# Performance work log

Hardware: AMD Instinct MI355X
Metric: run time of the kernel (lower is better)

Reference implementation:

```python
import jax, jax.numpy as jnp
import numpy as np

B, T, D = 4, 2048, 1024
GROUPS = 32
EPS = 1e-5
THETA = 10000.0


def _rope(x):
    # lucidrains RotaryEmbedding: interleaved pairs over the full dim
    d = x.shape[-1]
    t = x.shape[-2]
    inv_freq = 1.0 / (THETA ** (jnp.arange(0, d, 2, dtype=jnp.float32) / d))  # [d/2]
    freqs = jnp.arange(t, dtype=jnp.float32)[:, None] * inv_freq[None, :]      # [T, d/2]
    cos = jnp.cos(freqs).astype(x.dtype)
    sin = jnp.sin(freqs).astype(x.dtype)
    x1 = x[..., 0::2]
    x2 = x[..., 1::2]
    r1 = x1 * cos - x2 * sin
    r2 = x1 * sin + x2 * cos
    return jnp.stack([r1, r2], axis=-1).reshape(x.shape)


def _group_norm(z, weight, bias):
    # z: [N, C]; normalize per group of C//GROUPS channels
    n, c = z.shape
    zg = z.reshape(n, GROUPS, c // GROUPS)
    mean = zg.mean(axis=-1, keepdims=True)
    var = zg.var(axis=-1, keepdims=True)
    zg = (zg - mean) * jax.lax.rsqrt(var + EPS)
    return zg.reshape(n, c) * weight + bias


def setup_inputs() -> dict:
    key = jax.random.key(0)
    k1, k2, k3 = jax.random.split(key, 3)
    x = jax.random.normal(k1, (B, T, D), dtype=jnp.float32)
    W_in = jax.random.normal(k2, (D, 3 * D), dtype=jnp.float32) * (1.0 / np.sqrt(D))
    b_in = jax.random.normal(k3, (3 * D,), dtype=jnp.float32) * 0.02
    gn_weight = jnp.ones((D,), dtype=jnp.float32)
    gn_bias = jnp.zeros((D,), dtype=jnp.float32)
    return {"x": x, "W_in": W_in, "b_in": b_in, "gn_weight": gn_weight, "gn_bias": gn_bias}


def reference(x, W_in, b_in, gn_weight, gn_bias):
    b, t, c = x.shape
    qkv = x @ W_in + b_in                    # [B,T,3D]
    Q, K, V = jnp.split(qkv, 3, axis=-1)
    Q = jax.nn.relu(_rope(Q))
    K = jax.nn.relu(_rope(K))
    V = jax.nn.relu(V)
    A = jnp.einsum('btd,bsd->bts', Q, K)     # [B,T,T], no softmax
    y = jnp.einsum('bts,bsd->btd', A, V)     # [B,T,D]
    y = _group_norm(y.reshape(-1, c), gn_weight, gn_bias).reshape(b, t, c)
    # faithful to original: transpose(-2,-1).reshape(B,T,dim)
    return jnp.swapaxes(y, -2, -1).reshape(b, t, c)
```

## Files before the change

### kernel.cpp

```cpp
#include <hip/hip_runtime.h>


typedef unsigned short u16;
typedef __attribute__((ext_vector_type(8))) unsigned short u16x8;
typedef __attribute__((ext_vector_type(4))) float fx4;
typedef __attribute__((ext_vector_type(8))) __bf16 bfx8;

#define TP 129

__device__ __forceinline__ u16 f2bh(float v) {
  unsigned u = __float_as_uint(v);
  return (u16)((u + 0x7FFFu + ((u >> 16) & 1u)) >> 16);
}
__device__ __forceinline__ fx4 mfma16(bfx8 a, bfx8 b, fx4 c) {
  return __builtin_amdgcn_mfma_f32_16x16x32_bf16(a, b, c, 0, 0, 0);
}

__device__ __forceinline__ void gload16(const u16* g, u16* l) {
  __builtin_amdgcn_global_load_lds(
      (const __attribute__((address_space(1))) unsigned int*)(const void*)g,
      (__attribute__((address_space(3))) unsigned int*)(void*)l, 16, 0, 0);
}

__device__ __forceinline__ bfx8 ldsw(const u16* lds, int row, int slot) {
  const char* p = (const char*)lds + row * 128 + ((slot ^ (row & 7)) << 4);
  return __builtin_bit_cast(bfx8, *reinterpret_cast<const u16x8*>(p));
}

__device__ __forceinline__ void stage4(const u16* __restrict__ A,
                                       size_t rowBase, int stride, int k0,
                                       u16* lds, int w, int lane) {
#pragma unroll
  for (int i = 0; i < 4; ++i) {
    int c = ((w * 4 + i) << 6) + lane;
    int r = c >> 3, s = c & 7;
    int t = s ^ (r & 7);
    const u16* src = A + (rowBase + (size_t)r) * (size_t)stride + k0 + (t << 3);
    gload16(src, lds + ((w * 4 + i) << 9));
  }
}

__device__ inline void gemm_core_pipe(const u16* __restrict__ A, size_t aBase, int aStr,
                                      const u16* __restrict__ B, size_t bBase, int bStr, int K,
                                      u16* sA0, u16* sB0, u16* sA1, u16* sB1,
                                      fx4 acc[4][4], int w, int lane) {
  int wm = (w >> 1) * 64, wn = (w & 1) * 64;
  int lr = lane & 15, lk = lane >> 4;
  stage4(A, aBase, aStr, 0, sA0, w, lane);
  stage4(B, bBase, bStr, 0, sB0, w, lane);
  int NT = K >> 6;
  for (int t = 0; t < NT; ++t) {
    u16* cA = (t & 1) ? sA1 : sA0;
    u16* cB = (t & 1) ? sB1 : sB0;
    if (t + 1 < NT) {
      u16* nA = (t & 1) ? sA0 : sA1;
      u16* nB = (t & 1) ? sB0 : sB1;
      stage4(A, aBase, aStr, (t + 1) << 6, nA, w, lane);
      stage4(B, bBase, bStr, (t + 1) << 6, nB, w, lane);
      asm volatile("s_waitcnt vmcnt(8)" ::: "memory");
    } else {
      asm volatile("s_waitcnt vmcnt(0)" ::: "memory");
    }
    __builtin_amdgcn_s_barrier();
    __builtin_amdgcn_sched_barrier(0);
    bfx8 a[8], b[8];
#pragma unroll
    for (int h = 0; h < 2; ++h)
#pragma unroll
      for (int i = 0; i < 4; ++i) {
        a[h * 4 + i] = ldsw(cA, wm + i * 16 + lr, h * 4 + lk);
        b[h * 4 + i] = ldsw(cB, wn + i * 16 + lr, h * 4 + lk);
      }
    asm volatile("s_waitcnt lgkmcnt(0)" ::: "memory");
    __builtin_amdgcn_sched_barrier(0);
    __builtin_amdgcn_s_barrier();
#pragma unroll
    for (int h = 0; h < 2; ++h)
#pragma unroll
      for (int mi = 0; mi < 4; ++mi)
#pragma unroll
        for (int ni = 0; ni < 4; ++ni)
          acc[mi][ni] = mfma16(a[h * 4 + mi], b[h * 4 + ni], acc[mi][ni]);
  }
}

__global__ void k_ropetab(float2* __restrict__ tabTI, float2* __restrict__ tabIT) {
  int idx = blockIdx.x * 256 + threadIdx.x;
  int t, i;
  if (blockIdx.y == 0) {
    t = idx >> 9;
    i = idx & 511;
  } else {
    i = idx >> 11;
    t = idx & 2047;
  }
  float invf = exp2f(-(float)i * (13.287712379549449f / 512.f));
  float ang = (float)t * invf, s, c;
  sincosf(ang, &s, &c);
  if (blockIdx.y == 0)
    tabTI[idx] = make_float2(c, s);
  else
    tabIT[idx] = make_float2(c, s);
}

__global__ void k_transW(const float* __restrict__ W, u16* __restrict__ WTh) {
  __shared__ float tile[32][33];
  int n0 = blockIdx.x * 32, k0 = blockIdx.y * 32;
  int tid = threadIdx.x;
  int c = tid & 31, r4 = tid >> 5;
#pragma unroll
  for (int it = 0; it < 4; ++it) {
    int r = r4 + it * 8;
    tile[r][c] = W[(size_t)(k0 + r) * 3072 + n0 + c];
  }
  __syncthreads();
#pragma unroll
  for (int it = 0; it < 4; ++it) {
    int r = r4 + it * 8;
    WTh[(size_t)(n0 + r) * 1024 + k0 + c] = f2bh(tile[c][r]);
  }
}

__global__ void k_castX(const float* __restrict__ x, u16* __restrict__ xh) {
  size_t i = ((size_t)blockIdx.x * 256 + threadIdx.x) * 8;
  fx4 v0 = *reinterpret_cast<const fx4*>(x + i);
  fx4 v1 = *reinterpret_cast<const fx4*>(x + i + 4);
  u16x8 h;
#pragma unroll
  for (int j = 0; j < 4; ++j) {
    h[j] = f2bh(v0[j]);
    h[4 + j] = f2bh(v1[j]);
  }
  *reinterpret_cast<u16x8*>(xh + i) = h;
}

__global__ __launch_bounds__(256) void k_gemm1f(const u16* __restrict__ xh,
                                                const u16* __restrict__ WTh,
                                                const float* __restrict__ b_in,
                                                const float2* __restrict__ tabTI,
                                                const float2* __restrict__ tabIT,
                                                u16* __restrict__ Qh, u16* __restrict__ Kth,
                                                u16* __restrict__ Vth) {
  __shared__ __align__(16) float shbuf[128 * TP];
  u16* sA0 = (u16*)shbuf;
  u16* sB0 = sA0 + 128 * 64;
  u16* sA1 = sB0 + 128 * 64;
  u16* sB1 = sA1 + 128 * 64;
  int bid = blockIdx.x;
  int xcd = bid & 7, idx = bid >> 3;
  int mt = (xcd << 3) + (idx & 7), nt = idx >> 3;
  int m0 = mt << 7, n0 = nt << 7;
  int tid = threadIdx.x, lane = tid & 63, w = tid >> 6;
  int wm = (w >> 1) * 64, wn = (w & 1) * 64;
  int lr = lane & 15, lk = lane >> 4;
  fx4 acc[4][4];
#pragma unroll
  for (int i = 0; i < 4; ++i)
#pragma unroll
    for (int j = 0; j < 4; ++j) acc[i][j] = fx4{0.f, 0.f, 0.f, 0.f};

  gemm_core_pipe(xh, (size_t)m0, 1024, WTh, (size_t)n0, 1024, 1024,
                 sA0, sB0, sA1, sB1, acc, w, lane);

  float bv[4];
#pragma unroll
  for (int ni = 0; ni < 4; ++ni) bv[ni] = b_in[n0 + wn + ni * 16 + lr];
  __syncthreads();
#pragma unroll
  for (int mi = 0; mi < 4; ++mi)
#pragma unroll
    for (int ni = 0; ni < 4; ++ni)
#pragma unroll
      for (int r = 0; r < 4; ++r)
        shbuf[(wn + ni * 16 + lr) * TP + wm + mi * 16 + lk * 4 + r] = acc[mi][ni][r] + bv[ni];
  __syncthreads();

  int part = n0 >> 10;
  int d0 = n0 - (part << 10);
  int bb = m0 >> 11, tb = m0 & 2047;
  int rl0 = tid >> 4;
  int cc = (tid & 15) * 8;

  if (part == 2) {
#pragma unroll
    for (int pass = 0; pass < 8; ++pass) {
      int rl = rl0 + pass * 16;
      u16x8 o;
#pragma unroll
      for (int j = 0; j < 8; ++j) o[j] = f2bh(fmaxf(shbuf[rl * TP + cc + j], 0.f));
      *reinterpret_cast<u16x8*>(Vth + (((size_t)(bb << 10) + d0 + rl) << 11) + tb + cc) = o;
    }
  } else if (part == 1) {
#pragma unroll
    for (int pass = 0; pass < 8; ++pass) {
      int rl = rl0 + pass * 16;
      int d = d0 + rl;
      const float2* tp = tabIT + ((size_t)(d >> 1) << 11) + tb + cc;
      const float* e = shbuf + (rl & ~1) * TP + cc;
      const float* oo = shbuf + (rl | 1) * TP + cc;
      int isOdd = d & 1;
      u16x8 o;
#pragma unroll
      for (int j = 0; j < 8; ++j) {
        float2 cs = tp[j];
        float x1 = e[j], x2 = oo[j];
        float v = isOdd ? (x1 * cs.y + x2 * cs.x) : (x1 * cs.x - x2 * cs.y);
        o[j] = f2bh(fmaxf(v, 0.f));
      }
      *reinterpret_cast<u16x8*>(Kth + (((size_t)(bb << 10) + d) << 11) + tb + cc) = o;
    }
  } else {
#pragma unroll
    for (int pass = 0; pass < 8; ++pass) {
      int rl = rl0 + pass * 16;
      int m = m0 + rl, t = m & 2047;
      const float2* tp = tabTI + ((size_t)t << 9) + ((d0 + cc) >> 1);
      u16x8 o;
#pragma unroll
      for (int jp = 0; jp < 4; ++jp) {
        float x1 = shbuf[(cc + 2 * jp) * TP + rl];
        float x2 = shbuf[(cc + 2 * jp + 1) * TP + rl];
        float2 cs = tp[jp];
        o[2 * jp] = f2bh(fmaxf(x1 * cs.x - x2 * cs.y, 0.f));
        o[2 * jp + 1] = f2bh(fmaxf(x1 * cs.y + x2 * cs.x, 0.f));
      }
      *reinterpret_cast<u16x8*>(Qh + ((size_t)m << 10) + d0 + cc) = o;
    }
  }
}

__global__ __launch_bounds__(256) void k_gemm2(const u16* __restrict__ Kth, const u16* __restrict__ Vth,
                                               u16* __restrict__ KtVTh) {
  __shared__ u16 smem[4 * 128 * 64];
  u16* sA0 = smem;
  u16* sB0 = sA0 + 128 * 64;
  u16* sA1 = sB0 + 128 * 64;
  u16* sB1 = sA1 + 128 * 64;
  fx4 acc[4][4];
#pragma unroll
  for (int i = 0; i < 4; ++i)
#pragma unroll
    for (int j = 0; j < 4; ++j) acc[i][j] = fx4{0.f, 0.f, 0.f, 0.f};
  int b = blockIdx.z;
  int m0 = blockIdx.x << 7, n0 = blockIdx.y << 7;
  int tid = threadIdx.x, lane = tid & 63, w = tid >> 6;
  const u16* Ab = Kth + ((size_t)b << 21);
  const u16* Bb = Vth + ((size_t)b << 21);
  gemm_core_pipe(Ab, (size_t)m0, 2048, Bb, (size_t)n0, 2048, 2048,
                 sA0, sB0, sA1, sB1, acc, w, lane);
  int wm = (w >> 1) * 64, wn = (w & 1) * 64, lr = lane & 15, lk = lane >> 4;
#pragma unroll
  for (int mi = 0; mi < 4; ++mi)
#pragma unroll
    for (int ni = 0; ni < 4; ++ni)
#pragma unroll
      for (int r = 0; r < 4; ++r) {
        int m = m0 + wm + mi * 16 + lk * 4 + r;
        int n = n0 + wn + ni * 16 + lr;
        KtVTh[((size_t)b << 20) + ((size_t)n << 10) + m] = f2bh(acc[mi][ni][r]);
      }
}

__global__ __launch_bounds__(256) void k_gemm3g(const u16* __restrict__ Qh, const u16* __restrict__ KtVTh,
                                                const float* __restrict__ gw, const float* __restrict__ gb,
                                                float* __restrict__ out) {
  __shared__ u16 smem[4 * 128 * 64];
  u16* sA0 = smem;
  u16* sB0 = sA0 + 128 * 64;
  u16* sA1 = sB0 + 128 * 64;
  u16* sB1 = sA1 + 128 * 64;
  fx4 acc[4][4];
#pragma unroll
  for (int i = 0; i < 4; ++i)
#pragma unroll
    for (int j = 0; j < 4; ++j) acc[i][j] = fx4{0.f, 0.f, 0.f, 0.f};
  int b = blockIdx.z;
  int m0 = blockIdx.x << 7, n0 = blockIdx.y << 7;
  int tid = threadIdx.x, lane = tid & 63, w = tid >> 6;
  gemm_core_pipe(Qh, (size_t)(b * 2048 + m0), 1024, KtVTh + ((size_t)b << 20), (size_t)n0, 1024,
                 1024, sA0, sB0, sA1, sB1, acc, w, lane);
  int wm = (w >> 1) * 64, wn = (w & 1) * 64, lr = lane & 15, lk = lane >> 4;
  float wv[4], bvv[4];
#pragma unroll
  for (int ni = 0; ni < 4; ++ni) {
    int n = n0 + wn + ni * 16 + lr;
    wv[ni] = gw[n];
    bvv[ni] = gb[n];
  }
#pragma unroll
  for (int mi = 0; mi < 4; ++mi) {
    fx4 o0, o1, o2, o3;
#pragma unroll
    for (int r = 0; r < 4; ++r) {
      float v0 = acc[mi][0][r], v1 = acc[mi][1][r], v2 = acc[mi][2][r], v3 = acc[mi][3][r];
      float sA2 = v0 + v1, sB2 = v2 + v3;
#pragma unroll
      for (int mk = 1; mk <= 8; mk <<= 1) {
        sA2 += __shfl_xor(sA2, mk);
        sB2 += __shfl_xor(sB2, mk);
      }
      float mA = sA2 * (1.f / 32.f), mB = sB2 * (1.f / 32.f);
      float dA = (v0 - mA) * (v0 - mA) + (v1 - mA) * (v1 - mA);
      float dB = (v2 - mB) * (v2 - mB) + (v3 - mB) * (v3 - mB);
#pragma unroll
      for (int mk = 1; mk <= 8; mk <<= 1) {
        dA += __shfl_xor(dA, mk);
        dB += __shfl_xor(dB, mk);
      }
      float rA = rsqrtf(dA * (1.f / 32.f) + 1e-5f);
      float rB = rsqrtf(dB * (1.f / 32.f) + 1e-5f);
      o0[r] = (v0 - mA) * rA * wv[0] + bvv[0];
      o1[r] = (v1 - mA) * rA * wv[1] + bvv[1];
      o2[r] = (v2 - mB) * rB * wv[2] + bvv[2];
      o3[r] = (v3 - mB) * rB * wv[3] + bvv[3];
    }
    int mbase = m0 + wm + mi * 16 + lk * 4;
#pragma unroll
    for (int ni = 0; ni < 4; ++ni) {
      int n = n0 + wn + ni * 16 + lr;
      fx4 ov = (ni == 0) ? o0 : (ni == 1) ? o1 : (ni == 2) ? o2 : o3;
      *reinterpret_cast<fx4*>(out + (((size_t)(b << 10) + n) << 11) + mbase) = ov;
    }
  }
}

extern "C" void kernel_launch(void* const* d_in, const int* in_sizes, int n_in,
                              void* d_out, int out_size, void* d_ws, size_t ws_size,
                              hipStream_t stream) {
  const float* x = (const float*)d_in[0];
  const float* W = (const float*)d_in[1];
  const float* b_in = (const float*)d_in[2];
  const float* gnw = (const float*)d_in[3];
  const float* gnb = (const float*)d_in[4];
  float* out = (float*)d_out;
  char* ws = (char*)d_ws;

  u16* xh = (u16*)(ws + 0);
  u16* WTh = (u16*)(ws + 16777216);
  u16* Qh = (u16*)(ws + 23068672);
  u16* Kth = (u16*)(ws + 39845888);
  u16* Vth = (u16*)(ws + 56623104);
  u16* KtVTh = (u16*)(ws + 73400320);
  float2* tabTI = (float2*)(ws + 81788928);
  float2* tabIT = (float2*)(ws + 90177536);

  k_ropetab<<<dim3(4096, 2), 256, 0, stream>>>(tabTI, tabIT);
  k_transW<<<dim3(96, 32), 256, 0, stream>>>(W, WTh);
  k_castX<<<4096, 256, 0, stream>>>(x, xh);
  k_gemm1f<<<1536, 256, 0, stream>>>(xh, WTh, b_in, tabTI, tabIT, Qh, Kth, Vth);
  k_gemm2<<<dim3(8, 8, 4), 256, 0, stream>>>(Kth, Vth, KtVTh);
  k_gemm3g<<<dim3(16, 8, 4), 256, 0, stream>>>(Qh, KtVTh, gnw, gnb, out);
}
```

Baseline: 146.1 us.

## Merge prep kernels into one launch and remap GEMM blocks per XCD

Folds the rope-table, weight-transpose and x-cast kernels into a single launch that picks its role from the block index, removing two kernel launches and their gaps. The two attention GEMMs switch to a 1D grid whose block ids are remapped so each XCD handles one batch and a contiguous set of tiles. This is meant to improve L2 locality on MI355X's per-XCD caches. The merged prep kernel allocates a shared-memory tile for every block, even those that do not use it.

```diff
diff --git a/kernel.cpp b/kernel.cpp
--- a/kernel.cpp
+++ b/kernel.cpp
@@ -84,54 +84,56 @@
   }
 }
 
-__global__ void k_ropetab(float2* __restrict__ tabTI, float2* __restrict__ tabIT) {
-  int idx = blockIdx.x * 256 + threadIdx.x;
-  int t, i;
-  if (blockIdx.y == 0) {
-    t = idx >> 9;
-    i = idx & 511;
+__global__ void k_prep(const float* __restrict__ x, const float* __restrict__ W,
+                       u16* __restrict__ xh, u16* __restrict__ WTh,
+                       float2* __restrict__ tabTI, float2* __restrict__ tabIT) {
+  __shared__ float tile[32][33];
+  int bid = blockIdx.x, tid = threadIdx.x;
+  if (bid < 4096) {
+    size_t i = ((size_t)bid * 256 + tid) * 8;
+    fx4 v0 = *reinterpret_cast<const fx4*>(x + i);
+    fx4 v1 = *reinterpret_cast<const fx4*>(x + i + 4);
+    u16x8 h;
+#pragma unroll
+    for (int j = 0; j < 4; ++j) {
+      h[j] = f2bh(v0[j]);
+      h[4 + j] = f2bh(v1[j]);
+    }
+    *reinterpret_cast<u16x8*>(xh + i) = h;
+  } else if (bid < 7168) {
+    int idx = bid - 4096;
+    int n0 = (idx % 96) * 32, k0 = (idx / 96) * 32;
+    int c = tid & 31, r4 = tid >> 5;
+#pragma unroll
+    for (int it = 0; it < 4; ++it) {
+      int r = r4 + it * 8;
+      tile[r][c] = W[(size_t)(k0 + r) * 3072 + n0 + c];
+    }
+    __syncthreads();
+#pragma unroll
+    for (int it = 0; it < 4; ++it) {
+      int r = r4 + it * 8;
+      WTh[(size_t)(n0 + r) * 1024 + k0 + c] = f2bh(tile[c][r]);
+    }
   } else {
-    i = idx >> 11;
-    t = idx & 2047;
-  }
-  float invf = exp2f(-(float)i * (13.287712379549449f / 512.f));
-  float ang = (float)t * invf, s, c;
-  sincosf(ang, &s, &c);
-  if (blockIdx.y == 0)
-    tabTI[idx] = make_float2(c, s);
-  else
-    tabIT[idx] = make_float2(c, s);
-}
-
-__global__ void k_transW(const float* __restrict__ W, u16* __restrict__ WTh) {
-  __shared__ float tile[32][33];
-  int n0 = blockIdx.x * 32, k0 = blockIdx.y * 32;
-  int tid = threadIdx.x;
-  int c = tid & 31, r4 = tid >> 5;
-#pragma unroll
-  for (int it = 0; it < 4; ++it) {
-    int r = r4 + it * 8;
-    tile[r][c] = W[(size_t)(k0 + r) * 3072 + n0 + c];
-  }
-  __syncthreads();
-#pragma unroll
-  for (int it = 0; it < 4; ++it) {
-    int r = r4 + it * 8;
-    WTh[(size_t)(n0 + r) * 1024 + k0 + c] = f2bh(tile[c][r]);
-  }
-}
-
-__global__ void k_castX(const float* __restrict__ x, u16* __restrict__ xh) {
-  size_t i = ((size_t)blockIdx.x * 256 + threadIdx.x) * 8;
-  fx4 v0 = *reinterpret_cast<const fx4*>(x + i);
-  fx4 v1 = *reinterpret_cast<const fx4*>(x + i + 4);
-  u16x8 h;
-#pragma unroll
-  for (int j = 0; j < 4; ++j) {
-    h[j] = f2bh(v0[j]);
-    h[4 + j] = f2bh(v1[j]);
-  }
-  *reinterpret_cast<u16x8*>(xh + i) = h;
+    int half = (bid - 7168) >> 12;
+    int idx = ((bid - 7168) & 4095) * 256 + tid;
+    int t, i;
+    if (half == 0) {
+      t = idx >> 9;
+      i = idx & 511;
+    } else {
+      i = idx >> 11;
+      t = idx & 2047;
+    }
+    float invf = exp2f(-(float)i * (13.287712379549449f / 512.f));
+    float ang = (float)t * invf, s, c;
+    sincosf(ang, &s, &c);
+    if (half == 0)
+      tabTI[idx] = make_float2(c, s);
+    else
+      tabIT[idx] = make_float2(c, s);
+  }
 }
 
 __global__ __launch_bounds__(256) void k_gemm1f(const u16* __restrict__ xh,
@@ -241,8 +243,11 @@
   for (int i = 0; i < 4; ++i)
 #pragma unroll
     for (int j = 0; j < 4; ++j) acc[i][j] = fx4{0.f, 0.f, 0.f, 0.f};
-  int b = blockIdx.z;
-  int m0 = blockIdx.x << 7, n0 = blockIdx.y << 7;
+  int bid = blockIdx.x;
+  int xcd = bid & 7, idx = bid >> 3;
+  int b = xcd >> 1;
+  int mt = (xcd & 1) * 4 + (idx & 3), nt = idx >> 2;
+  int m0 = mt << 7, n0 = nt << 7;
   int tid = threadIdx.x, lane = tid & 63, w = tid >> 6;
   const u16* Ab = Kth + ((size_t)b << 21);
   const u16* Bb = Vth + ((size_t)b << 21);
@@ -274,8 +279,11 @@
   for (int i = 0; i < 4; ++i)
 #pragma unroll
     for (int j = 0; j < 4; ++j) acc[i][j] = fx4{0.f, 0.f, 0.f, 0.f};
-  int b = blockIdx.z;
-  int m0 = blockIdx.x << 7, n0 = blockIdx.y << 7;
+  int bid = blockIdx.x;
+  int xcd = bid & 7, idx = bid >> 3;
+  int b = xcd >> 1;
+  int mt = (xcd & 1) * 8 + (idx & 7), nt = idx >> 3;
+  int m0 = mt << 7, n0 = nt << 7;
   int tid = threadIdx.x, lane = tid & 63, w = tid >> 6;
   gemm_core_pipe(Qh, (size_t)(b * 2048 + m0), 1024, KtVTh + ((size_t)b << 20), (size_t)n0, 1024,
                  1024, sA0, sB0, sA1, sB1, acc, w, lane);
@@ -344,10 +352,8 @@
   float2* tabTI = (float2*)(ws + 81788928);
   float2* tabIT = (float2*)(ws + 90177536);
 
-  k_ropetab<<<dim3(4096, 2), 256, 0, stream>>>(tabTI, tabIT);
-  k_transW<<<dim3(96, 32), 256, 0, stream>>>(W, WTh);
-  k_castX<<<4096, 256, 0, stream>>>(x, xh);
+  k_prep<<<15360, 256, 0, stream>>>(x, W, xh, WTh, tabTI, tabIT);
   k_gemm1f<<<1536, 256, 0, stream>>>(xh, WTh, b_in, tabTI, tabIT, Qh, Kth, Vth);
-  k_gemm2<<<dim3(8, 8, 4), 256, 0, stream>>>(Kth, Vth, KtVTh);
-  k_gemm3g<<<dim3(16, 8, 4), 256, 0, stream>>>(Qh, KtVTh, gnw, gnb, out);
-}
+  k_gemm2<<<256, 256, 0, stream>>>(Kth, Vth, KtVTh);
+  k_gemm3g<<<512, 256, 0, stream>>>(Qh, KtVTh, gnw, gnb, out);
+}
```

After: 140.3 us. 1.04x faster.
